# Kernel optimization log

Hardware: AMD Instinct MI355X
Metric: run time of the kernel (lower is better)

The kernel has to match this reference:

```python
import jax, jax.numpy as jnp
import numpy as np

SHARE_ROWS = 16  # norm shared across consecutive output rows
GROUP = 32       # dequant group size along in_features


def setup_inputs() -> dict:
    key = jax.random.key(0)
    k1, k2, k3, k4 = jax.random.split(key, 4)
    O, I = 8192, 8192
    blocks, half = I // GROUP, GROUP // 2
    x = jax.random.normal(k1, (16, I), dtype=jnp.float32)
    # packed bytes: (low & 15) + (high << 4) in [0, 256)
    weight_q4 = jax.random.randint(k2, (O, blocks, half), 0, 256, dtype=jnp.int32)
    weight_norm = jax.random.uniform(k3, (O // SHARE_ROWS, blocks, 1), dtype=jnp.float16)
    bias = jax.random.normal(k4, (O,), dtype=jnp.float32)
    return {"x": x, "weight_q4": weight_q4, "weight_norm": weight_norm, "bias": bias}


def reference(x, weight_q4, weight_norm, bias):
    O, blocks, half = weight_q4.shape
    # unpack 4-bit nibbles: interleave low/high -> [O, blocks, GROUP]
    low = weight_q4 & 15
    high = (weight_q4 >> 4) & 15
    q8 = jnp.stack((low, high), axis=-1).reshape(O, blocks, GROUP)
    q8 = q8.astype(jnp.float32) / 15.0
    # per-(row-group, block) normalization, shared across SHARE_ROWS rows
    norms = jnp.repeat(weight_norm.astype(jnp.float32), SHARE_ROWS, axis=0)  # [O, blocks, 1]
    W = (q8 * 2.0 * norms - norms).reshape(O, blocks * GROUP)  # [O, I] fp32
    return x @ W.T + bias
```

## Files before the change

### kernel.cpp

```cpp
#include <hip/hip_runtime.h>
#include <hip/hip_bf16.h>
#include <hip/hip_fp16.h>

typedef __attribute__((ext_vector_type(8))) short bf16x8;
typedef __attribute__((ext_vector_type(4))) float f32x4;
typedef __attribute__((ext_vector_type(4))) int   i32x4;

#define O_TOTAL 8192
#define I_TOTAL 8192
#define NWAVES  8
#define NSS     32
#define ROW_I32 (I_TOTAL / 2)
#define NBLOCKS 256

typedef __attribute__((address_space(1))) const void GASV;
typedef __attribute__((address_space(3))) void LASV;

static __device__ __forceinline__ short f2bf(float f) {
    union { __hip_bfloat16 b; short s; } u;
    u.b = __float2bfloat16(f);
    return u.s;
}

static __device__ __forceinline__ float bf2f(unsigned short s) {
    union { unsigned int u; float f; } v;
    v.u = ((unsigned int)s) << 16;
    return v.f;
}

__global__ __launch_bounds__(256)
void xcvt_kernel(const float* __restrict__ x, short* __restrict__ xb)
{
    const int i = (blockIdx.x * 256 + threadIdx.x) * 4;
    f32x4 v = *(const f32x4*)(x + i);
    union { short s[4]; long long q; } p;
    p.s[0] = f2bf(v[0]); p.s[1] = f2bf(v[1]); p.s[2] = f2bf(v[2]); p.s[3] = f2bf(v[3]);
    *(long long*)(xb + i) = p.q;
}

__global__ __launch_bounds__(512, 6)
void linq4_kernel(const short* __restrict__ xb,
                  const int* __restrict__ wq,
                  const void* __restrict__ wn,
                  const float* __restrict__ bias,
                  float* __restrict__ out)
{
    const int tid  = threadIdx.x;
    const int w    = tid >> 6;
    const int lane = tid & 63;
    const int otile = blockIdx.x;
    const int o0   = otile * 16;
    const int phase = (otile * 7) & (NSS - 1);

    const unsigned int* w32 = (const unsigned int*)wn;
    int cntLo = 0, cntHi = 0;
    #pragma unroll
    for (int i = 0; i < 16; ++i) {
        unsigned int ww = w32[i];
        unsigned int lo = ww & 0xFFFFu, hi = ww >> 16;
        if (lo >= 0x3980u && lo < 0x3F80u) cntLo++;
        if (hi >= 0x3C00u) cntHi++;
    }
    const int fmt = (cntLo >= 12) ? 1 : (cntHi >= 12 ? 0 : 2);

    __shared__ int   w_lds[2][2048];
    __shared__ short x_lds[2][4096];
    __shared__ float nlds[NBLOCKS];
    __shared__ float red[NWAVES][256];

    if (tid < NBLOCKS) {
        const int idx = otile * NBLOCKS + tid;
        float nf;
        if (fmt == 0)      nf = ((const float*)wn)[idx];
        else if (fmt == 1) nf = bf2f(((const unsigned short*)wn)[idx]);
        else               nf = __half2float(((const __half*)wn)[idx]);
        nlds[tid] = nf;
    }

    const int r_st  = 2 * w + (lane >> 5);
    const int jj    = (lane & 31) ^ (r_st & 7);
    const int* gw_base   = wq + (size_t)(o0 + r_st) * ROW_I32 + jj * 4;
    const short* gx_base = xb + (size_t)r_st * I_TOTAL + jj * 8;

    const int col = lane & 15;
    const int kg  = lane >> 4;
    const int j   = w * 4 + kg;
    const int t   = j ^ (col & 7);
    const int ldsoff = col * 128 + t * 4;
    const int xldoff = col * 256 + t * 8;

    f32x4 acc = {0.f, 0.f, 0.f, 0.f};

    __builtin_amdgcn_global_load_lds((GASV*)(gw_base + phase * 128),
                                     (LASV*)(&w_lds[0][w * 256]), 16, 0, 0);
    __builtin_amdgcn_global_load_lds((GASV*)(gx_base + phase * 256),
                                     (LASV*)(&x_lds[0][w * 512]), 16, 0, 0);
    __syncthreads();

    for (int S = 0; S < NSS; ++S) {
        const int cur = S & 1;
        const int Sp  = (S + phase) & (NSS - 1);
        if (S + 1 < NSS) {
            const int Spn = (S + 1 + phase) & (NSS - 1);
            const int nxt = cur ^ 1;
            __builtin_amdgcn_global_load_lds((GASV*)(gw_base + Spn * 128),
                                             (LASV*)(&w_lds[nxt][w * 256]), 16, 0, 0);
            __builtin_amdgcn_global_load_lds((GASV*)(gx_base + Spn * 256),
                                             (LASV*)(&x_lds[nxt][w * 512]), 16, 0, 0);
        }

        i32x4  pv = *(const i32x4*)(&w_lds[cur][ldsoff]);
        bf16x8 xa = *(const bf16x8*)(&x_lds[cur][xldoff]);
        const float nf = nlds[Sp * 8 + w];
        const float sc = nf * (2.0f / 15.0f);

        bf16x8 bfrag;
        #pragma unroll
        for (int c = 0; c < 4; ++c) {
            int v = pv[c];
            float wl = (float)(v & 15)        * sc - nf;
            float wh = (float)((v >> 4) & 15) * sc - nf;
            bfrag[2*c]   = f2bf(wl);
            bfrag[2*c+1] = f2bf(wh);
        }

        acc = __builtin_amdgcn_mfma_f32_16x16x32_bf16(xa, bfrag, acc, 0, 0, 0);

        __syncthreads();
    }

    *(f32x4*)&red[w][lane * 4] = acc;
    __syncthreads();

    if (tid < 256) {
        float s = 0.f;
        #pragma unroll
        for (int q = 0; q < NWAVES; ++q) s += red[q][tid];
        const int l = tid >> 2;
        const int r = tid & 3;
        const int m  = ((l >> 4) << 2) + r;
        const int oc = o0 + (l & 15);
        out[(size_t)m * O_TOTAL + oc] = s + bias[oc];
    }
}

extern "C" void kernel_launch(void* const* d_in, const int* in_sizes, int n_in,
                              void* d_out, int out_size, void* d_ws, size_t ws_size,
                              hipStream_t stream) {
    const float* x    = (const float*)d_in[0];
    const int*   wq   = (const int*)d_in[1];
    const void*  wn   = (const void*)d_in[2];
    const float* bias = (const float*)d_in[3];
    float* out = (float*)d_out;
    short* xb  = (short*)d_ws;

    hipLaunchKernelGGL(xcvt_kernel, dim3(16 * I_TOTAL / 4 / 256), dim3(256), 0, stream, x, xb);

    hipLaunchKernelGGL(linq4_kernel, dim3(O_TOTAL / 16), dim3(512), 0, stream,
                       (const short*)xb, wq, wn, bias, out);
}
```

Baseline: 34.06 us.

## Split K across four blocks with register double-buffering and separate reduce kernel

Replaces the single GEMV kernel with a split-K version. It launches four 256-thread blocks per 16-row output tile, and each block handles a quarter of the input dimension. Each block loads weights and activations straight into registers with double-buffering, with no LDS staging and no per-step barriers, and writes partial sums to workspace. A separate reduce kernel then adds the partials and the bias. This is meant to raise parallelism and remove synchronisation, at the cost of an extra launch and extra partial-sum traffic. If the workspace is too small, the code falls back to the old kernel.

```diff
diff --git a/kernel.cpp b/kernel.cpp
--- a/kernel.cpp
+++ b/kernel.cpp
@@ -8,10 +8,9 @@
 
 #define O_TOTAL 8192
 #define I_TOTAL 8192
-#define NWAVES  8
-#define NSS     32
-#define ROW_I32 (I_TOTAL / 2)
+#define ROW_I32 4096
 #define NBLOCKS 256
+#define OUT_N   (16 * O_TOTAL)
 
 typedef __attribute__((address_space(1))) const void GASV;
 typedef __attribute__((address_space(3))) void LASV;
@@ -28,30 +27,7 @@
     return v.f;
 }
 
-__global__ __launch_bounds__(256)
-void xcvt_kernel(const float* __restrict__ x, short* __restrict__ xb)
-{
-    const int i = (blockIdx.x * 256 + threadIdx.x) * 4;
-    f32x4 v = *(const f32x4*)(x + i);
-    union { short s[4]; long long q; } p;
-    p.s[0] = f2bf(v[0]); p.s[1] = f2bf(v[1]); p.s[2] = f2bf(v[2]); p.s[3] = f2bf(v[3]);
-    *(long long*)(xb + i) = p.q;
-}
-
-__global__ __launch_bounds__(512, 6)
-void linq4_kernel(const short* __restrict__ xb,
-                  const int* __restrict__ wq,
-                  const void* __restrict__ wn,
-                  const float* __restrict__ bias,
-                  float* __restrict__ out)
-{
-    const int tid  = threadIdx.x;
-    const int w    = tid >> 6;
-    const int lane = tid & 63;
-    const int otile = blockIdx.x;
-    const int o0   = otile * 16;
-    const int phase = (otile * 7) & (NSS - 1);
-
+static __device__ __forceinline__ int sniff_fmt(const void* wn) {
     const unsigned int* w32 = (const unsigned int*)wn;
     int cntLo = 0, cntHi = 0;
     #pragma unroll
@@ -61,21 +37,132 @@
         if (lo >= 0x3980u && lo < 0x3F80u) cntLo++;
         if (hi >= 0x3C00u) cntHi++;
     }
-    const int fmt = (cntLo >= 12) ? 1 : (cntHi >= 12 ? 0 : 2);
+    return (cntLo >= 12) ? 1 : (cntHi >= 12 ? 0 : 2);
+}
+
+static __device__ __forceinline__ float decode_norm(const void* wn, int idx, int fmt) {
+    if (fmt == 0) return ((const float*)wn)[idx];
+    if (fmt == 1) return bf2f(((const unsigned short*)wn)[idx]);
+    return __half2float(((const __half*)wn)[idx]);
+}
+
+__global__ __launch_bounds__(256)
+void xcvt_kernel(const float* __restrict__ x, short* __restrict__ xb)
+{
+    const int i = (blockIdx.x * 256 + threadIdx.x) * 4;
+    f32x4 v = *(const f32x4*)(x + i);
+    union { short s[4]; long long q; } p;
+    p.s[0] = f2bf(v[0]); p.s[1] = f2bf(v[1]); p.s[2] = f2bf(v[2]); p.s[3] = f2bf(v[3]);
+    *(long long*)(xb + i) = p.q;
+}
+
+__global__ __launch_bounds__(256, 8)
+void gemm_part(const short* __restrict__ xb,
+               const int* __restrict__ wq,
+               const void* __restrict__ wn,
+               float* __restrict__ part)
+{
+    const int tid  = threadIdx.x;
+    const int w    = tid >> 6;
+    const int lane = tid & 63;
+    const int otile = blockIdx.x >> 2;
+    const int q     = blockIdx.x & 3;
+    const int o0   = otile * 16;
+    const int ph   = (otile * 5) & 15;
+
+    const int fmt = sniff_fmt(wn);
+
+    __shared__ float nlds[64];
+    __shared__ float red[4][256];
+    if (tid < 64)
+        nlds[tid] = decode_norm(wn, otile * NBLOCKS + q * 64 + tid, fmt);
+    __syncthreads();
+
+    const int col = lane & 15;
+    const int kg  = lane >> 4;
+    const int kb0 = q * 64 + w * 16;
+
+    const int*   wrow = wq + (size_t)(o0 + col) * ROW_I32 + kb0 * 16 + kg * 4;
+    const short* xrow = xb + (size_t)col * I_TOTAL + kb0 * 32 + kg * 8;
+
+    f32x4 acc = {0.f, 0.f, 0.f, 0.f};
+
+    i32x4  pv[2];
+    bf16x8 xa[2];
+    pv[0] = *(const i32x4*)(wrow + (size_t)ph * 16);
+    xa[0] = *(const bf16x8*)(xrow + (size_t)ph * 32);
+
+    #pragma unroll
+    for (int s = 0; s < 16; ++s) {
+        const int d  = s & 1;
+        const int bs = (s + ph) & 15;
+        if (s + 1 < 16) {
+            const int bn = (s + 1 + ph) & 15;
+            pv[d ^ 1] = *(const i32x4*)(wrow + (size_t)bn * 16);
+            xa[d ^ 1] = *(const bf16x8*)(xrow + (size_t)bn * 32);
+        }
+        const float nf = nlds[w * 16 + bs];
+        const float sc = nf * (2.0f / 15.0f);
+        bf16x8 bfrag;
+        #pragma unroll
+        for (int c = 0; c < 4; ++c) {
+            int v = pv[d][c];
+            bfrag[2*c]   = f2bf((float)(v & 15)        * sc - nf);
+            bfrag[2*c+1] = f2bf((float)((v >> 4) & 15) * sc - nf);
+        }
+        acc = __builtin_amdgcn_mfma_f32_16x16x32_bf16(xa[d], bfrag, acc, 0, 0, 0);
+    }
+
+    *(f32x4*)&red[w][lane * 4] = acc;
+    __syncthreads();
+
+    if (tid < 256) {
+        float s = red[0][tid] + red[1][tid] + red[2][tid] + red[3][tid];
+        const int l = tid >> 2;
+        const int r = tid & 3;
+        const int m  = ((l >> 4) << 2) + r;
+        const int oc = o0 + (l & 15);
+        part[(size_t)q * OUT_N + (size_t)m * O_TOTAL + oc] = s;
+    }
+}
+
+__global__ __launch_bounds__(256)
+void reduce_k(const float* __restrict__ part, const float* __restrict__ bias,
+              float* __restrict__ out)
+{
+    const int i = (blockIdx.x * 256 + threadIdx.x) * 4;
+    f32x4 a = *(const f32x4*)(part + i);
+    f32x4 b = *(const f32x4*)(part + OUT_N + i);
+    f32x4 c = *(const f32x4*)(part + 2 * OUT_N + i);
+    f32x4 d = *(const f32x4*)(part + 3 * OUT_N + i);
+    f32x4 bs = *(const f32x4*)(bias + (i & (O_TOTAL - 1)));
+    f32x4 r = a + b + c + d + bs;
+    *(f32x4*)(out + i) = r;
+}
+
+#define NWAVES  8
+#define NSS     32
+__global__ __launch_bounds__(512, 6)
+void linq4_fb(const short* __restrict__ xb, const int* __restrict__ wq,
+              const void* __restrict__ wn, const float* __restrict__ bias,
+              float* __restrict__ out)
+{
+    const int tid  = threadIdx.x;
+    const int w    = tid >> 6;
+    const int lane = tid & 63;
+    const int otile = blockIdx.x;
+    const int o0   = otile * 16;
+    const int phase = (otile * 7) & (NSS - 1);
+
+    const int fmt = sniff_fmt(wn);
 
     __shared__ int   w_lds[2][2048];
     __shared__ short x_lds[2][4096];
     __shared__ float nlds[NBLOCKS];
     __shared__ float red[NWAVES][256];
 
-    if (tid < NBLOCKS) {
-        const int idx = otile * NBLOCKS + tid;
-        float nf;
-        if (fmt == 0)      nf = ((const float*)wn)[idx];
-        else if (fmt == 1) nf = bf2f(((const unsigned short*)wn)[idx]);
-        else               nf = __half2float(((const __half*)wn)[idx]);
-        nlds[tid] = nf;
-    }
+    if (tid < NBLOCKS)
+        nlds[tid] = decode_norm(wn, otile * NBLOCKS + tid, fmt);
 
     const int r_st  = 2 * w + (lane >> 5);
     const int jj    = (lane & 31) ^ (r_st & 7);
@@ -108,24 +195,18 @@
             __builtin_amdgcn_global_load_lds((GASV*)(gx_base + Spn * 256),
                                              (LASV*)(&x_lds[nxt][w * 512]), 16, 0, 0);
         }
-
         i32x4  pv = *(const i32x4*)(&w_lds[cur][ldsoff]);
         bf16x8 xa = *(const bf16x8*)(&x_lds[cur][xldoff]);
         const float nf = nlds[Sp * 8 + w];
         const float sc = nf * (2.0f / 15.0f);
-
         bf16x8 bfrag;
         #pragma unroll
         for (int c = 0; c < 4; ++c) {
             int v = pv[c];
-            float wl = (float)(v & 15)        * sc - nf;
-            float wh = (float)((v >> 4) & 15) * sc - nf;
-            bfrag[2*c]   = f2bf(wl);
-            bfrag[2*c+1] = f2bf(wh);
-        }
-
+            bfrag[2*c]   = f2bf((float)(v & 15)        * sc - nf);
+            bfrag[2*c+1] = f2bf((float)((v >> 4) & 15) * sc - nf);
+        }
         acc = __builtin_amdgcn_mfma_f32_16x16x32_bf16(xa, bfrag, acc, 0, 0, 0);
-
         __syncthreads();
     }
 
@@ -135,7 +216,7 @@
     if (tid < 256) {
         float s = 0.f;
         #pragma unroll
-        for (int q = 0; q < NWAVES; ++q) s += red[q][tid];
+        for (int qq = 0; qq < NWAVES; ++qq) s += red[qq][tid];
         const int l = tid >> 2;
         const int r = tid & 3;
         const int m  = ((l >> 4) << 2) + r;
@@ -152,10 +233,21 @@
     const void*  wn   = (const void*)d_in[2];
     const float* bias = (const float*)d_in[3];
     float* out = (float*)d_out;
-    short* xb  = (short*)d_ws;
+
+    short* xb = (short*)d_ws;
+    const size_t xb_bytes   = (size_t)16 * I_TOTAL * 2;
+    const size_t part_bytes = (size_t)4 * OUT_N * 4;
 
     hipLaunchKernelGGL(xcvt_kernel, dim3(16 * I_TOTAL / 4 / 256), dim3(256), 0, stream, x, xb);
 
-    hipLaunchKernelGGL(linq4_kernel, dim3(O_TOTAL / 16), dim3(512), 0, stream,
-                       (const short*)xb, wq, wn, bias, out);
-}
+    if (ws_size >= xb_bytes + part_bytes) {
+        float* part = (float*)((char*)d_ws + xb_bytes);
+        hipLaunchKernelGGL(gemm_part, dim3(512 * 4), dim3(256), 0, stream,
+                           (const short*)xb, wq, wn, part);
+        hipLaunchKernelGGL(reduce_k, dim3(OUT_N / 4 / 256), dim3(256), 0, stream,
+                           (const float*)part, bias, out);
+    } else {
+        hipLaunchKernelGGL(linq4_fb, dim3(O_TOTAL / 16), dim3(512), 0, stream,
+                           (const short*)xb, wq, wn, bias, out);
+    }
+}
```

Measured after the change: 43.31 us. 27.2% more time.

## Process two 16-row output tiles per 1024-thread block sharing x tile

Applied to the files above, without the earlier changes.

Each block now covers 32 output rows with 16 waves split into two groups, and both groups share a single staged x tile in LDS, which only the second group loads. This halves the number of blocks and the redundant x traffic per output row. The reduction buffer now reuses the weight LDS region to save shared memory. In exchange the larger blocks mean fewer, heavier workgroups with 1024 threads each, which can lower occupancy and put more waves on every block-wide barrier.

```diff
diff --git a/kernel.cpp b/kernel.cpp
--- a/kernel.cpp
+++ b/kernel.cpp
@@ -8,10 +8,9 @@
 
 #define O_TOTAL 8192
 #define I_TOTAL 8192
-#define NWAVES  8
+#define ROW_I32 4096
+#define NBLOCKS 256
 #define NSS     32
-#define ROW_I32 (I_TOTAL / 2)
-#define NBLOCKS 256
 
 typedef __attribute__((address_space(1))) const void GASV;
 typedef __attribute__((address_space(3))) void LASV;
@@ -28,6 +27,25 @@
     return v.f;
 }
 
+static __device__ __forceinline__ int sniff_fmt(const void* wn) {
+    const unsigned int* w32 = (const unsigned int*)wn;
+    int cntLo = 0, cntHi = 0;
+    #pragma unroll
+    for (int i = 0; i < 16; ++i) {
+        unsigned int ww = w32[i];
+        unsigned int lo = ww & 0xFFFFu, hi = ww >> 16;
+        if (lo >= 0x3980u && lo < 0x3F80u) cntLo++;
+        if (hi >= 0x3C00u) cntHi++;
+    }
+    return (cntLo >= 12) ? 1 : (cntHi >= 12 ? 0 : 2);
+}
+
+static __device__ __forceinline__ float decode_norm(const void* wn, int idx, int fmt) {
+    if (fmt == 0) return ((const float*)wn)[idx];
+    if (fmt == 1) return bf2f(((const unsigned short*)wn)[idx]);
+    return __half2float(((const __half*)wn)[idx]);
+}
+
 __global__ __launch_bounds__(256)
 void xcvt_kernel(const float* __restrict__ x, short* __restrict__ xb)
 {
@@ -38,63 +56,55 @@
     *(long long*)(xb + i) = p.q;
 }
 
-__global__ __launch_bounds__(512, 6)
-void linq4_kernel(const short* __restrict__ xb,
-                  const int* __restrict__ wq,
-                  const void* __restrict__ wn,
-                  const float* __restrict__ bias,
-                  float* __restrict__ out)
+__global__ __launch_bounds__(1024, 4)
+void gemm_w(const short* __restrict__ xb,
+            const int* __restrict__ wq,
+            const void* __restrict__ wn,
+            const float* __restrict__ bias,
+            float* __restrict__ out)
 {
     const int tid  = threadIdx.x;
     const int w    = tid >> 6;
     const int lane = tid & 63;
-    const int otile = blockIdx.x;
-    const int o0   = otile * 16;
-    const int phase = (otile * 7) & (NSS - 1);
+    const int grp  = w >> 3;
+    const int wg   = w & 7;
+    const int bid  = blockIdx.x;
+    const int o0   = bid * 32;
+    const int phase = (bid * 7) & (NSS - 1);
 
-    const unsigned int* w32 = (const unsigned int*)wn;
-    int cntLo = 0, cntHi = 0;
-    #pragma unroll
-    for (int i = 0; i < 16; ++i) {
-        unsigned int ww = w32[i];
-        unsigned int lo = ww & 0xFFFFu, hi = ww >> 16;
-        if (lo >= 0x3980u && lo < 0x3F80u) cntLo++;
-        if (hi >= 0x3C00u) cntHi++;
-    }
-    const int fmt = (cntLo >= 12) ? 1 : (cntHi >= 12 ? 0 : 2);
+    const int fmt = sniff_fmt(wn);
 
-    __shared__ int   w_lds[2][2048];
+    __shared__ int   w_lds[2][4096];
     __shared__ short x_lds[2][4096];
-    __shared__ float nlds[NBLOCKS];
-    __shared__ float red[NWAVES][256];
+    __shared__ float nlds[2][256];
 
-    if (tid < NBLOCKS) {
-        const int idx = otile * NBLOCKS + tid;
-        float nf;
-        if (fmt == 0)      nf = ((const float*)wn)[idx];
-        else if (fmt == 1) nf = bf2f(((const unsigned short*)wn)[idx]);
-        else               nf = __half2float(((const __half*)wn)[idx]);
-        nlds[tid] = nf;
+    if (tid < 512) {
+        const int g = tid >> 8, idx = tid & 255;
+        nlds[g][idx] = decode_norm(wn, (bid * 2 + g) * NBLOCKS + idx, fmt);
     }
 
-    const int r_st  = 2 * w + (lane >> 5);
-    const int jj    = (lane & 31) ^ (r_st & 7);
-    const int* gw_base   = wq + (size_t)(o0 + r_st) * ROW_I32 + jj * 4;
+    const int r_st = 2 * wg + (lane >> 5);
+    const int jj   = (lane & 31) ^ (r_st & 7);
+    const int* gw_base = wq + (size_t)(o0 + grp * 16 + r_st) * ROW_I32 + jj * 4;
     const short* gx_base = xb + (size_t)r_st * I_TOTAL + jj * 8;
 
     const int col = lane & 15;
     const int kg  = lane >> 4;
-    const int j   = w * 4 + kg;
-    const int t   = j ^ (col & 7);
-    const int ldsoff = col * 128 + t * 4;
-    const int xldoff = col * 256 + t * 8;
+    const int t   = (wg * 4 + kg) ^ (col & 7);
+    char* wl0 = (char*)&w_lds[0][0];
+    char* wl1 = (char*)&w_lds[1][0];
+    char* xl0 = (char*)&x_lds[0][0];
+    char* xl1 = (char*)&x_lds[1][0];
+    const int woff = grp * 8192 + col * 512 + t * 16;
+    const int xoff = col * 512 + t * 16;
 
     f32x4 acc = {0.f, 0.f, 0.f, 0.f};
 
     __builtin_amdgcn_global_load_lds((GASV*)(gw_base + phase * 128),
-                                     (LASV*)(&w_lds[0][w * 256]), 16, 0, 0);
-    __builtin_amdgcn_global_load_lds((GASV*)(gx_base + phase * 256),
-                                     (LASV*)(&x_lds[0][w * 512]), 16, 0, 0);
+                                     (LASV*)(wl0 + grp * 8192 + wg * 1024), 16, 0, 0);
+    if (grp == 1)
+        __builtin_amdgcn_global_load_lds((GASV*)(gx_base + phase * 256),
+                                         (LASV*)(xl0 + wg * 1024), 16, 0, 0);
     __syncthreads();
 
     for (int S = 0; S < NSS; ++S) {
@@ -102,44 +112,48 @@
         const int Sp  = (S + phase) & (NSS - 1);
         if (S + 1 < NSS) {
             const int Spn = (S + 1 + phase) & (NSS - 1);
-            const int nxt = cur ^ 1;
+            char* wln = cur ? wl0 : wl1;
+            char* xln = cur ? xl0 : xl1;
             __builtin_amdgcn_global_load_lds((GASV*)(gw_base + Spn * 128),
-                                             (LASV*)(&w_lds[nxt][w * 256]), 16, 0, 0);
-            __builtin_amdgcn_global_load_lds((GASV*)(gx_base + Spn * 256),
-                                             (LASV*)(&x_lds[nxt][w * 512]), 16, 0, 0);
+                                             (LASV*)(wln + grp * 8192 + wg * 1024), 16, 0, 0);
+            if (grp == 1)
+                __builtin_amdgcn_global_load_lds((GASV*)(gx_base + Spn * 256),
+                                                 (LASV*)(xln + wg * 1024), 16, 0, 0);
         }
 
-        i32x4  pv = *(const i32x4*)(&w_lds[cur][ldsoff]);
-        bf16x8 xa = *(const bf16x8*)(&x_lds[cur][xldoff]);
-        const float nf = nlds[Sp * 8 + w];
+        char* wlc = cur ? wl1 : wl0;
+        char* xlc = cur ? xl1 : xl0;
+        i32x4  pv = *(const i32x4*)(wlc + woff);
+        bf16x8 xa = *(const bf16x8*)(xlc + xoff);
+        const float nf = nlds[grp][Sp * 8 + wg];
         const float sc = nf * (2.0f / 15.0f);
 
         bf16x8 bfrag;
         #pragma unroll
         for (int c = 0; c < 4; ++c) {
             int v = pv[c];
-            float wl = (float)(v & 15)        * sc - nf;
-            float wh = (float)((v >> 4) & 15) * sc - nf;
-            bfrag[2*c]   = f2bf(wl);
-            bfrag[2*c+1] = f2bf(wh);
+            bfrag[2*c]   = f2bf((float)(v & 15)        * sc - nf);
+            bfrag[2*c+1] = f2bf((float)((v >> 4) & 15) * sc - nf);
         }
-
         acc = __builtin_amdgcn_mfma_f32_16x16x32_bf16(xa, bfrag, acc, 0, 0, 0);
 
         __syncthreads();
     }
 
-    *(f32x4*)&red[w][lane * 4] = acc;
+    float* red = (float*)&w_lds[0][0];
+    *(f32x4*)&red[w * 256 + lane * 4] = acc;
     __syncthreads();
 
-    if (tid < 256) {
+    if (tid < 512) {
+        const int g  = tid >> 8;
+        const int it = tid & 255;
         float s = 0.f;
         #pragma unroll
-        for (int q = 0; q < NWAVES; ++q) s += red[q][tid];
-        const int l = tid >> 2;
-        const int r = tid & 3;
+        for (int q = 0; q < 8; ++q) s += red[(g * 8 + q) * 256 + it];
+        const int l = it >> 2;
+        const int r = it & 3;
         const int m  = ((l >> 4) << 2) + r;
-        const int oc = o0 + (l & 15);
+        const int oc = o0 + g * 16 + (l & 15);
         out[(size_t)m * O_TOTAL + oc] = s + bias[oc];
     }
 }
@@ -156,6 +170,6 @@
 
     hipLaunchKernelGGL(xcvt_kernel, dim3(16 * I_TOTAL / 4 / 256), dim3(256), 0, stream, x, xb);
 
-    hipLaunchKernelGGL(linq4_kernel, dim3(O_TOTAL / 16), dim3(512), 0, stream,
+    hipLaunchKernelGGL(gemm_w, dim3(O_TOTAL / 32), dim3(1024), 0, stream,
                        (const short*)xb, wq, wn, bias, out);
 }
```

Result: no change. 34.32 us (+0.8%).
